# Optimization experiments

Hardware: AMD Instinct MI355X
Metric: run time of the kernel (lower is better)

## Reference

```python
import jax, jax.numpy as jnp
import numpy as np

IN_F = 4096
OUT_F = 4096
RANK = 16
NUM_SLOTS = 32
ALPHA = 1.0


def setup_inputs() -> dict:
    key = jax.random.key(0)
    k_x, k_w, k_b, k_a, k_bm, k_idx = jax.random.split(key, 6)
    x = jax.random.normal(k_x, (8, 2048, IN_F), dtype=jnp.float32)
    weight = jax.random.normal(k_w, (OUT_F, IN_F), dtype=jnp.float32) * (1.0 / np.sqrt(IN_F))
    bias = jax.random.normal(k_b, (OUT_F,), dtype=jnp.float32) * 0.01
    lora_A = jax.random.normal(k_a, (NUM_SLOTS, IN_F, RANK), dtype=jnp.float32) * 1e-4
    lora_B = jax.random.normal(k_bm, (NUM_SLOTS, RANK, OUT_F), dtype=jnp.float32) * 1e-4
    lora_indices = jax.random.randint(k_idx, (8,), 0, NUM_SLOTS)
    return {"x": x, "weight": weight, "bias": bias, "lora_A": lora_A,
            "lora_B": lora_B, "lora_indices": lora_indices}


def reference(x, weight, bias, lora_A, lora_B, lora_indices):
    # base linear: x @ W.T + b
    out = jnp.einsum('bsd,od->bso', x, weight) + bias
    # per-sample LoRA slot gather + low-rank bmm chain
    chosen_A = lora_A[lora_indices]          # [B, in, r]
    chosen_B = lora_B[lora_indices]          # [B, r, out]
    inter = jnp.einsum('bsd,bdr->bsr', x, chosen_A)       # [B, S, r]
    out_lora = jnp.einsum('bsr,bro->bso', inter, chosen_B)  # [B, S, out]
    return out + ALPHA * out_lora
```

## Files before the change

### kernel.cpp

```cpp
#include <hip/hip_runtime.h>
#include <hip/hip_bf16.h>


#define M_TOT 16384
#define K_TOT 4096
#define N_TOT 4096
#define RANK 16
#define NT2 64

typedef __attribute__((ext_vector_type(8))) short bf16x8;
typedef __attribute__((ext_vector_type(4))) float f32x4;

__device__ __forceinline__ unsigned short f2bf(float f) {
  unsigned int u = __builtin_bit_cast(unsigned int, f);
  u += 0x7fffu + ((u >> 16) & 1u);
  return (unsigned short)(u >> 16);
}

__global__ void cvt_bf16_kernel(const float* __restrict__ src,
                                unsigned short* __restrict__ dst, int n4) {
  int i = blockIdx.x * blockDim.x + threadIdx.x;
  const int stride = gridDim.x * blockDim.x;
  for (; i < n4; i += stride) {
    const float4 v = reinterpret_cast<const float4*>(src)[i];
    ushort4 o;
    o.x = f2bf(v.x); o.y = f2bf(v.y); o.z = f2bf(v.z); o.w = f2bf(v.w);
    reinterpret_cast<ushort4*>(dst)[i] = o;
  }
}

__global__ __launch_bounds__(256) void fused_xcvt_inter_kernel(
    const float* __restrict__ x,
    const float* __restrict__ loraA,
    const int* __restrict__ idx,
    unsigned short* __restrict__ xb,
    float* __restrict__ inter) {
  const int lane = threadIdx.x & 63;
  const int wv = threadIdx.x >> 6;
  const int m0 = blockIdx.x * 64 + wv * 16;
  const int slot = idx[m0 >> 11];
  const int q = lane >> 4;
  const int c = lane & 15;
  const float* __restrict__ xrow = x + (size_t)(m0 + c) * K_TOT + q * 8;
  unsigned short* __restrict__ xbrow = xb + (size_t)(m0 + c) * K_TOT + q * 8;
  const float* __restrict__ Abase = loraA + (size_t)slot * K_TOT * RANK + c;

  f32x4 acc = (f32x4){0.f, 0.f, 0.f, 0.f};
#pragma unroll 4
  for (int kt = 0; kt < K_TOT; kt += 32) {
    const float4 xv0 = *reinterpret_cast<const float4*>(xrow + kt);
    const float4 xv1 = *reinterpret_cast<const float4*>(xrow + kt + 4);
    bf16x8 af;
    af[0] = (short)f2bf(xv0.x); af[1] = (short)f2bf(xv0.y);
    af[2] = (short)f2bf(xv0.z); af[3] = (short)f2bf(xv0.w);
    af[4] = (short)f2bf(xv1.x); af[5] = (short)f2bf(xv1.y);
    af[6] = (short)f2bf(xv1.z); af[7] = (short)f2bf(xv1.w);
    *reinterpret_cast<bf16x8*>(xbrow + kt) = af;
    const float* __restrict__ Ak = Abase + (size_t)(kt + q * 8) * RANK;
    bf16x8 bfr;
#pragma unroll
    for (int j = 0; j < 8; ++j) bfr[j] = (short)f2bf(Ak[(size_t)j * RANK]);
    acc = __builtin_amdgcn_mfma_f32_16x16x32_bf16(af, bfr, acc, 0, 0, 0);
  }
#pragma unroll
  for (int i = 0; i < 4; ++i)
    inter[(size_t)(m0 + q * 4 + i) * RANK + c] = acc[i];
}

__device__ __forceinline__ void gload16(const void* g, void* l) {
  __builtin_amdgcn_global_load_lds(
      (const __attribute__((address_space(1))) unsigned int*)g,
      (__attribute__((address_space(3))) unsigned int*)l, 16, 0, 0);
}

#define GBARRIER() asm volatile("s_barrier" ::: "memory")
#define RD(p) (*reinterpret_cast<const bf16x8*>(p))

__global__ __launch_bounds__(512, 2) void gemm_fused_kernel(
    const unsigned short* __restrict__ xb,
    const unsigned short* __restrict__ wb,
    const float* __restrict__ bias,
    const float* __restrict__ inter,
    const float* __restrict__ loraB,
    const int* __restrict__ idx,
    float* __restrict__ out) {
  __shared__ unsigned short lds[2][32768];
  char* ldsB = (char*)&lds[0][0];

  const int tid = threadIdx.x;
  const int lane = tid & 63;
  const int wv = tid >> 6;
  const int wr = wv >> 2;
  const int wc = wv & 3;

  const int bid = ((blockIdx.x & 7) << 7) | (blockIdx.x >> 3);
  const int m0 = (bid >> 4) << 8;
  const int n0 = (bid & 15) << 8;

  const int r0 = tid >> 3;
  const int scol = ((tid & 7) ^ (r0 & 7)) << 3;
  const unsigned short* xsrc = xb + (size_t)(m0 + r0) * K_TOT + scol;
  const unsigned short* wsrc = wb + (size_t)(n0 + r0) * K_TOT + scol;
  const int stg = tid << 4;

#define STAGE64(t)                                                       \
  do {                                                                   \
    const int _bo = (((t) & 1) << 16);                                   \
    const size_t _ko = (size_t)(t) * 64;                                 \
    gload16(xsrc + _ko,                        ldsB + _bo + stg);        \
    gload16(xsrc + (size_t)64  * K_TOT + _ko,  ldsB + _bo + 8192 + stg); \
    gload16(xsrc + (size_t)128 * K_TOT + _ko,  ldsB + _bo + 16384 + stg);\
    gload16(xsrc + (size_t)192 * K_TOT + _ko,  ldsB + _bo + 24576 + stg);\
    gload16(wsrc + _ko,                        ldsB + _bo + 32768 + stg);\
    gload16(wsrc + (size_t)64  * K_TOT + _ko,  ldsB + _bo + 40960 + stg);\
    gload16(wsrc + (size_t)128 * K_TOT + _ko,  ldsB + _bo + 49152 + stg);\
    gload16(wsrc + (size_t)192 * K_TOT + _ko,  ldsB + _bo + 57344 + stg);\
  } while (0)

  const int rl = lane & 15;
  const int q = lane >> 4;
  const int swz = rl & 7;
  const int aoff0 = (wr * 128 + rl) * 128 + ((q ^ swz) << 4);
  const int aoff1 = (wr * 128 + rl) * 128 + (((4 + q) ^ swz) << 4);
  const int boff0 = 32768 + (wc * 64 + rl) * 128 + ((q ^ swz) << 4);
  const int boff1 = 32768 + (wc * 64 + rl) * 128 + (((4 + q) ^ swz) << 4);

  f32x4 acc[8][4];
#pragma unroll
  for (int i = 0; i < 8; ++i)
#pragma unroll
    for (int j = 0; j < 4; ++j) acc[i][j] = (f32x4){0.f, 0.f, 0.f, 0.f};

  STAGE64(0);
  asm volatile("s_waitcnt vmcnt(0)" ::: "memory");
  GBARRIER();

#pragma unroll 1
  for (int t = 0; t < NT2; ++t) {
    const char* base = ldsB + ((t & 1) << 16);
    bf16x8 af[8], bfr0[4], bfr1[4];

#pragma unroll
    for (int nf = 0; nf < 4; ++nf) bfr0[nf] = RD(base + boff0 + nf * 2048);
#pragma unroll
    for (int mf = 0; mf < 8; ++mf) af[mf] = RD(base + aoff0 + mf * 2048);
#pragma unroll
    for (int nf = 0; nf < 4; ++nf) bfr1[nf] = RD(base + boff1 + nf * 2048);
    if (t < NT2 - 1) STAGE64(t + 1);

    asm volatile("s_waitcnt lgkmcnt(4)" ::: "memory");
    __builtin_amdgcn_sched_barrier(0);
#pragma unroll
    for (int mf = 0; mf < 8; ++mf)
#pragma unroll
      for (int nf = 0; nf < 4; ++nf)
        acc[mf][nf] = __builtin_amdgcn_mfma_f32_16x16x32_bf16(
            af[mf], bfr0[nf], acc[mf][nf], 0, 0, 0);
    __builtin_amdgcn_sched_barrier(0);

#pragma unroll
    for (int mf = 0; mf < 8; ++mf) af[mf] = RD(base + aoff1 + mf * 2048);
    asm volatile("s_waitcnt lgkmcnt(0)" ::: "memory");
    __builtin_amdgcn_sched_barrier(0);
#pragma unroll
    for (int mf = 0; mf < 8; ++mf)
#pragma unroll
      for (int nf = 0; nf < 4; ++nf)
        acc[mf][nf] = __builtin_amdgcn_mfma_f32_16x16x32_bf16(
            af[mf], bfr1[nf], acc[mf][nf], 0, 0, 0);
    __builtin_amdgcn_sched_barrier(0);

    asm volatile("s_waitcnt vmcnt(0)" ::: "memory");
    GBARRIER();
  }

  const int slot = idx[m0 >> 11];
  const float* __restrict__ Bmat = loraB + (size_t)slot * RANK * N_TOT;
  const int gn0 = n0 + wc * 64 + rl;

  float bcv[4][RANK];
  float bv[4];
#pragma unroll
  for (int nf = 0; nf < 4; ++nf) {
    const int gn = gn0 + nf * 16;
    bv[nf] = bias[gn];
#pragma unroll
    for (int p = 0; p < RANK; ++p) bcv[nf][p] = Bmat[(size_t)p * N_TOT + gn];
  }
#pragma unroll
  for (int mf = 0; mf < 8; ++mf) {
    const int gmb = m0 + wr * 128 + mf * 16 + (q << 2);
#pragma unroll
    for (int r = 0; r < 4; ++r) {
      const int gm = gmb + r;
      const float4* ivp = reinterpret_cast<const float4*>(inter + (size_t)gm * RANK);
      const float4 iv0 = ivp[0], iv1 = ivp[1], iv2 = ivp[2], iv3 = ivp[3];
      float* orow = out + (size_t)gm * N_TOT;
#pragma unroll
      for (int nf = 0; nf < 4; ++nf) {
        const float lora =
            iv0.x * bcv[nf][0]  + iv0.y * bcv[nf][1]  + iv0.z * bcv[nf][2]  + iv0.w * bcv[nf][3] +
            iv1.x * bcv[nf][4]  + iv1.y * bcv[nf][5]  + iv1.z * bcv[nf][6]  + iv1.w * bcv[nf][7] +
            iv2.x * bcv[nf][8]  + iv2.y * bcv[nf][9]  + iv2.z * bcv[nf][10] + iv2.w * bcv[nf][11] +
            iv3.x * bcv[nf][12] + iv3.y * bcv[nf][13] + iv3.z * bcv[nf][14] + iv3.w * bcv[nf][15];
        orow[gn0 + nf * 16] = acc[mf][nf][r] + bv[nf] + lora;
      }
    }
  }
#undef STAGE64
}

extern "C" void kernel_launch(void* const* d_in, const int* in_sizes, int n_in,
                              void* d_out, int out_size, void* d_ws, size_t ws_size,
                              hipStream_t stream) {
  const float* x     = (const float*)d_in[0];
  const float* w     = (const float*)d_in[1];
  const float* bias  = (const float*)d_in[2];
  const float* loraA = (const float*)d_in[3];
  const float* loraB = (const float*)d_in[4];
  const int*   idx   = (const int*)d_in[5];
  float* out = (float*)d_out;

  char* ws = (char*)d_ws;
  unsigned short* xb   = (unsigned short*)ws;
  unsigned short* wbuf = (unsigned short*)(ws + 134217728);
  float* inter = (float*)(ws + 134217728 + 33554432);

  fused_xcvt_inter_kernel<<<M_TOT / 64, 256, 0, stream>>>(x, loraA, idx, xb, inter);
  cvt_bf16_kernel<<<1024, 256, 0, stream>>>(w, wbuf, N_TOT * K_TOT / 4);
  gemm_fused_kernel<<<(M_TOT / 256) * (N_TOT / 256), 512, 0, stream>>>(
      xb, wbuf, bias, inter, loraB, idx, out);
}
```

Measured before the change: 704.0 us.

## Split-K the x-convert/LoRA-inter kernel and raise MFMA wave priority

The fused x-conversion and LoRA down-projection kernel now assigns one 16-row tile per block and splits the K dimension across its four waves, combining the partial results through shared memory. This launches four times as many blocks, so more memory parallelism is available for the bandwidth-bound pass over x. In the main GEMM, s_setprio wraps the MFMA bursts so waves issuing matrix math get scheduling priority over waves doing loads. The cost is an extra LDS reduction and a barrier in the first kernel.

```diff
diff --git a/kernel.cpp b/kernel.cpp
--- a/kernel.cpp
+++ b/kernel.cpp
@@ -35,19 +35,21 @@
     const int* __restrict__ idx,
     unsigned short* __restrict__ xb,
     float* __restrict__ inter) {
+  __shared__ float red[4][16][17];
   const int lane = threadIdx.x & 63;
-  const int wv = threadIdx.x >> 6;
-  const int m0 = blockIdx.x * 64 + wv * 16;
+  const int wq = threadIdx.x >> 6;
+  const int m0 = blockIdx.x * 16;
   const int slot = idx[m0 >> 11];
   const int q = lane >> 4;
   const int c = lane & 15;
-  const float* __restrict__ xrow = x + (size_t)(m0 + c) * K_TOT + q * 8;
-  unsigned short* __restrict__ xbrow = xb + (size_t)(m0 + c) * K_TOT + q * 8;
+  const int k0 = wq * 1024;
+  const float* __restrict__ xrow = x + (size_t)(m0 + c) * K_TOT + k0 + q * 8;
+  unsigned short* __restrict__ xbrow = xb + (size_t)(m0 + c) * K_TOT + k0 + q * 8;
   const float* __restrict__ Abase = loraA + (size_t)slot * K_TOT * RANK + c;
 
   f32x4 acc = (f32x4){0.f, 0.f, 0.f, 0.f};
 #pragma unroll 4
-  for (int kt = 0; kt < K_TOT; kt += 32) {
+  for (int kt = 0; kt < 1024; kt += 32) {
     const float4 xv0 = *reinterpret_cast<const float4*>(xrow + kt);
     const float4 xv1 = *reinterpret_cast<const float4*>(xrow + kt + 4);
     bf16x8 af;
@@ -56,15 +58,23 @@
     af[4] = (short)f2bf(xv1.x); af[5] = (short)f2bf(xv1.y);
     af[6] = (short)f2bf(xv1.z); af[7] = (short)f2bf(xv1.w);
     *reinterpret_cast<bf16x8*>(xbrow + kt) = af;
-    const float* __restrict__ Ak = Abase + (size_t)(kt + q * 8) * RANK;
+    const float* __restrict__ Ak = Abase + (size_t)(k0 + kt + q * 8) * RANK;
     bf16x8 bfr;
 #pragma unroll
     for (int j = 0; j < 8; ++j) bfr[j] = (short)f2bf(Ak[(size_t)j * RANK]);
     acc = __builtin_amdgcn_mfma_f32_16x16x32_bf16(af, bfr, acc, 0, 0, 0);
   }
 #pragma unroll
-  for (int i = 0; i < 4; ++i)
-    inter[(size_t)(m0 + q * 4 + i) * RANK + c] = acc[i];
+  for (int i = 0; i < 4; ++i) red[wq][q * 4 + i][c] = acc[i];
+  __syncthreads();
+  if (wq == 0) {
+#pragma unroll
+    for (int i = 0; i < 4; ++i) {
+      const int row = q * 4 + i;
+      inter[(size_t)(m0 + row) * RANK + c] =
+          red[0][row][c] + red[1][row][c] + red[2][row][c] + red[3][row][c];
+    }
+  }
 }
 
 __device__ __forceinline__ void gload16(const void* g, void* l) {
@@ -150,24 +160,28 @@
 
     asm volatile("s_waitcnt lgkmcnt(4)" ::: "memory");
     __builtin_amdgcn_sched_barrier(0);
+    __builtin_amdgcn_s_setprio(1);
 #pragma unroll
     for (int mf = 0; mf < 8; ++mf)
 #pragma unroll
       for (int nf = 0; nf < 4; ++nf)
         acc[mf][nf] = __builtin_amdgcn_mfma_f32_16x16x32_bf16(
             af[mf], bfr0[nf], acc[mf][nf], 0, 0, 0);
+    __builtin_amdgcn_s_setprio(0);
     __builtin_amdgcn_sched_barrier(0);
 
 #pragma unroll
     for (int mf = 0; mf < 8; ++mf) af[mf] = RD(base + aoff1 + mf * 2048);
     asm volatile("s_waitcnt lgkmcnt(0)" ::: "memory");
     __builtin_amdgcn_sched_barrier(0);
+    __builtin_amdgcn_s_setprio(1);
 #pragma unroll
     for (int mf = 0; mf < 8; ++mf)
 #pragma unroll
       for (int nf = 0; nf < 4; ++nf)
         acc[mf][nf] = __builtin_amdgcn_mfma_f32_16x16x32_bf16(
             af[mf], bfr1[nf], acc[mf][nf], 0, 0, 0);
+    __builtin_amdgcn_s_setprio(0);
     __builtin_amdgcn_sched_barrier(0);
 
     asm volatile("s_waitcnt vmcnt(0)" ::: "memory");
@@ -226,7 +240,7 @@
   unsigned short* wbuf = (unsigned short*)(ws + 134217728);
   float* inter = (float*)(ws + 134217728 + 33554432);
 
-  fused_xcvt_inter_kernel<<<M_TOT / 64, 256, 0, stream>>>(x, loraA, idx, xb, inter);
+  fused_xcvt_inter_kernel<<<M_TOT / 16, 256, 0, stream>>>(x, loraA, idx, xb, inter);
   cvt_bf16_kernel<<<1024, 256, 0, stream>>>(w, wbuf, N_TOT * K_TOT / 4);
   gemm_fused_kernel<<<(M_TOT / 256) * (N_TOT / 256), 512, 0, stream>>>(
       xb, wbuf, bias, inter, loraB, idx, out);
```

New measurement: 643.7 us, median of 2. 8.6% less time.
